# Kernel optimization log

Measured on AMD Instinct MI355X. Metric: run time of the kernel, lower is better.

Reference implementation:

```python
import jax, jax.numpy as jnp
import numpy as np

EPS = 1e-12

def _l2norm(v, axis):
    n = jnp.sqrt(jnp.sum(v * v, axis=axis, keepdims=True))
    return v / jnp.maximum(n, EPS)

def setup_inputs() -> dict:
    key = jax.random.key(0)
    k1, k2, k3, k4 = jax.random.split(key, 4)
    N, T, D, K = 8, 2048, 512, 64
    x = jax.random.normal(k1, (N, T, D), dtype=jnp.float32)
    W = jax.random.normal(k2, (K, D), dtype=jnp.float32) * (1.0 / np.sqrt(D))  # Conv1d(k=1) weight squeezed
    b = jax.random.normal(k3, (K,), dtype=jnp.float32) * 0.01
    centroids = jax.random.uniform(k4, (K, D), dtype=jnp.float32)
    return {"x": x, "W": W, "b": b, "centroids": centroids}

def reference(x, W, b, centroids):
    N, T, D = x.shape
    K = centroids.shape[0]
    # L2-normalize descriptors along feature dim
    xn = _l2norm(x, axis=2)                                  # [N,T,D]
    # Conv1d with kernel_size=1 == per-timestep linear: [N,K,T] logits over clusters
    logits = jnp.einsum('ntd,kd->nkt', xn, W) + b[None, :, None]
    a = jax.nn.softmax(logits, axis=1)                       # soft assignment over K
    # Algebraically equal to sum_t a[n,k,t] * (xn[n,t,:] - c[k,:])
    vlad = jnp.einsum('nkt,ntd->nkd', a, xn) \
         - jnp.sum(a, axis=2)[:, :, None] * centroids[None]  # [N,K,D]
    vlad = _l2norm(vlad, axis=2)                             # intra-normalize per cluster
    vlad = vlad.reshape(N, K * D)
    return _l2norm(vlad, axis=1)                             # global L2 normalize
```

## Files before the change

kernel.cpp:

```cpp
#include <hip/hip_runtime.h>
#include <math.h>

#define EPS 1e-12f
#define NN 8
#define TT 2048
#define DD 512
#define KK 64

typedef short short8 __attribute__((ext_vector_type(8)));
typedef float floatx4 __attribute__((ext_vector_type(4)));

__device__ __forceinline__ unsigned short f2bf(float f) {
    unsigned int u = __float_as_uint(f);
    u += 0x7FFFu + ((u >> 16) & 1u);
    return (unsigned short)(u >> 16);
}
__device__ __forceinline__ unsigned int pack2(float a, float b) {
    return (unsigned int)f2bf(a) | ((unsigned int)f2bf(b) << 16);
}


__global__ __launch_bounds__(256) void kA(const float* __restrict__ x,
                                          const float* __restrict__ W,
                                          const float* __restrict__ bias,
                                          unsigned short* __restrict__ xbT,
                                          unsigned short* __restrict__ aTs,
                                          float* __restrict__ asumP,
                                          float* __restrict__ norms) {
    __shared__ __align__(16) unsigned char smem[67584];
    unsigned short* sW = (unsigned short*)smem;
    unsigned short* sT = (unsigned short*)smem;
    float* sRed = (float*)(smem + 66560);

    const int tid = threadIdx.x;
    const int bid = blockIdx.x;
    const int w = tid >> 6, lane = tid & 63;
    const int l = lane & 15, q = lane >> 4;
    const int row0 = bid * 64 + w * 16;
    const int row = row0 + l;
    const int n = row0 >> 11;
    const int tl0 = row0 & (TT - 1);
    const int tblk = (bid * 64) & (TT - 1);

    const float* xr = x + (size_t)row * DD;
    short8 fragA[16];
    float ssq = 0.0f;
#pragma unroll
    for (int s = 0; s < 16; ++s) {
        float4 u0 = *(const float4*)(xr + s * 32 + q * 8);
        float4 u1 = *(const float4*)(xr + s * 32 + q * 8 + 4);
        ssq += u0.x*u0.x + u0.y*u0.y + u0.z*u0.z + u0.w*u0.w
             + u1.x*u1.x + u1.y*u1.y + u1.z*u1.z + u1.w*u1.w;
        uint4 pk;
        pk.x = pack2(u0.x, u0.y); pk.y = pack2(u0.z, u0.w);
        pk.z = pack2(u1.x, u1.y); pk.w = pack2(u1.z, u1.w);
        union { uint4 u; short8 s8; } cvt; cvt.u = pk;
        fragA[s] = cvt.s8;
    }

    {
        const int sp = tid >> 4, hp = (tid >> 2) & 3, qp = tid & 3;
        const float* wsrc = W + (size_t)(hp * 16) * DD + sp * 32 + qp * 8;
        unsigned short* wdst = sW + (size_t)tid * 128;
#pragma unroll
        for (int j = 0; j < 16; ++j) {
            float4 u0 = *(const float4*)(wsrc + (size_t)j * DD);
            float4 u1 = *(const float4*)(wsrc + (size_t)j * DD + 4);
            uint4 pk;
            pk.x = pack2(u0.x, u0.y); pk.y = pack2(u0.z, u0.w);
            pk.z = pack2(u1.x, u1.y); pk.w = pack2(u1.z, u1.w);
            *(uint4*)(wdst + j * 8) = pk;
        }
    }

    ssq += __shfl_xor(ssq, 16, 64);
    ssq += __shfl_xor(ssq, 32, 64);
    float st = 1.0f / fmaxf(sqrtf(ssq), EPS);

    __syncthreads();

    floatx4 acc[4];
#pragma unroll
    for (int h = 0; h < 4; ++h) acc[h] = floatx4{0.f, 0.f, 0.f, 0.f};
#pragma unroll
    for (int s = 0; s < 16; ++s) {
#pragma unroll
        for (int h = 0; h < 4; ++h) {
            short8 wf = *(const short8*)(sW + ((size_t)((s * 4 + h) * 64) + lane) * 8);
            acc[h] = __builtin_amdgcn_mfma_f32_16x16x32_bf16(fragA[s], wf, acc[h], 0, 0, 0);
        }
    }

    float sr[4];
#pragma unroll
    for (int r = 0; r < 4; ++r) sr[r] = __shfl(st, 4 * q + r, 64);
    float bj[4];
#pragma unroll
    for (int h = 0; h < 4; ++h) bj[h] = bias[h * 16 + l];

    float av[4][4];
#pragma unroll
    for (int r = 0; r < 4; ++r) {
        float v0 = acc[0][r] * sr[r] + bj[0], v1 = acc[1][r] * sr[r] + bj[1];
        float v2 = acc[2][r] * sr[r] + bj[2], v3 = acc[3][r] * sr[r] + bj[3];
        float m = fmaxf(fmaxf(v0, v1), fmaxf(v2, v3));
#pragma unroll
        for (int msk = 1; msk <= 8; msk <<= 1) m = fmaxf(m, __shfl_xor(m, msk, 64));
        float e0 = __expf(v0 - m), e1 = __expf(v1 - m), e2 = __expf(v2 - m), e3 = __expf(v3 - m);
        float ss = e0 + e1 + e2 + e3;
#pragma unroll
        for (int msk = 1; msk <= 8; msk <<= 1) ss += __shfl_xor(ss, msk, 64);
        float inv = 1.0f / ss;
        av[0][r] = e0 * inv; av[1][r] = e1 * inv; av[2][r] = e2 * inv; av[3][r] = e3 * inv;
    }

#pragma unroll
    for (int h = 0; h < 4; ++h) {
        uint2 p;
        p.x = pack2(av[h][0] * sr[0], av[h][1] * sr[1]);
        p.y = pack2(av[h][2] * sr[2], av[h][3] * sr[3]);
        *(uint2*)(aTs + ((size_t)(n * KK + h * 16 + l)) * TT + tl0 + 4 * q) = p;
    }

#pragma unroll
    for (int h = 0; h < 4; ++h) {
        float sh = av[h][0] + av[h][1] + av[h][2] + av[h][3];
        sh += __shfl_xor(sh, 16, 64);
        sh += __shfl_xor(sh, 32, 64);
        if (q == 0) sRed[w * 64 + h * 16 + l] = sh;
    }
    __syncthreads();
    if (tid < 64) {
        float s0 = sRed[tid] + sRed[64 + tid] + sRed[128 + tid] + sRed[192 + tid];
        asumP[(size_t)bid * 64 + tid] = s0;
    }

#pragma unroll
    for (int s = 0; s < 16; ++s)
        *(short8*)(sT + (size_t)(w * 16 + l) * 520 + s * 32 + q * 8) = fragA[s];
    __syncthreads();

#pragma unroll
    for (int c = 0; c < 2; ++c) {
        int d = tid + c * 256;
        const unsigned short* colb = sT + d;
        unsigned short* ob = xbT + ((size_t)(n * DD + d)) * TT + tblk;
#pragma unroll
        for (int jj = 0; jj < 8; ++jj) {
            uint4 pk;
            pk.x = (unsigned int)colb[(jj * 8 + 0) * 520] | ((unsigned int)colb[(jj * 8 + 1) * 520] << 16);
            pk.y = (unsigned int)colb[(jj * 8 + 2) * 520] | ((unsigned int)colb[(jj * 8 + 3) * 520] << 16);
            pk.z = (unsigned int)colb[(jj * 8 + 4) * 520] | ((unsigned int)colb[(jj * 8 + 5) * 520] << 16);
            pk.w = (unsigned int)colb[(jj * 8 + 6) * 520] | ((unsigned int)colb[(jj * 8 + 7) * 520] << 16);
            *(uint4*)(ob + jj * 8) = pk;
        }
    }

    if (bid == 0) { norms[tid] = 0.0f; norms[tid + 256] = 0.0f; }
}

__global__ __launch_bounds__(256) void kB(const unsigned short* __restrict__ xbT,
                                          const unsigned short* __restrict__ aTs,
                                          const float* __restrict__ asumP,
                                          const float* __restrict__ cent,
                                          float* __restrict__ vpre,
                                          float* __restrict__ norms) {
    __shared__ float sAs[16];
    const int tid = threadIdx.x;
    const int w = tid >> 6, lane = tid & 63;
    const int l = lane & 15, q = lane >> 4;
    const int bid = blockIdx.x;
    const int kq = bid >> 6, n = (bid >> 3) & 7, dq = bid & 7;
    const int k0 = kq * 16;
    const int dbase = dq * 64 + w * 16;

    if (tid < 16) sAs[tid] = 0.0f;
    __syncthreads();
    {
        const int kk = tid & 15, chunk = tid >> 4;
        float p = asumP[(size_t)(n * 32 + chunk) * 64 + k0 + kk]
                + asumP[(size_t)(n * 32 + 16 + chunk) * 64 + k0 + kk];
        p += __shfl_xor(p, 16, 64);
        p += __shfl_xor(p, 32, 64);
        if (q == 0) atomicAdd(&sAs[kk], p);
    }

    const unsigned short* ap = aTs + ((size_t)(n * KK + k0 + l)) * TT + q * 8;
    const unsigned short* bp = xbT + ((size_t)(n * DD + dbase + l)) * TT + q * 8;
    floatx4 a0 = {0.f, 0.f, 0.f, 0.f}, a1 = a0, a2 = a0, a3 = a0;
#pragma unroll
    for (int s = 0; s < 64; s += 4) {
        a0 = __builtin_amdgcn_mfma_f32_16x16x32_bf16(*(const short8*)(ap + (s + 0) * 32),
                                                     *(const short8*)(bp + (s + 0) * 32), a0, 0, 0, 0);
        a1 = __builtin_amdgcn_mfma_f32_16x16x32_bf16(*(const short8*)(ap + (s + 1) * 32),
                                                     *(const short8*)(bp + (s + 1) * 32), a1, 0, 0, 0);
        a2 = __builtin_amdgcn_mfma_f32_16x16x32_bf16(*(const short8*)(ap + (s + 2) * 32),
                                                     *(const short8*)(bp + (s + 2) * 32), a2, 0, 0, 0);
        a3 = __builtin_amdgcn_mfma_f32_16x16x32_bf16(*(const short8*)(ap + (s + 3) * 32),
                                                     *(const short8*)(bp + (s + 3) * 32), a3, 0, 0, 0);
    }
    floatx4 acc;
#pragma unroll
    for (int r = 0; r < 4; ++r) acc[r] = (a0[r] + a1[r]) + (a2[r] + a3[r]);

    __syncthreads();

    const int d = dbase + l;
#pragma unroll
    for (int r = 0; r < 4; ++r) {
        int k = k0 + 4 * q + r;
        float val = acc[r] - sAs[4 * q + r] * cent[(size_t)k * DD + d];
        vpre[((size_t)(n * KK + k)) * DD + d] = val;
        float s2 = val * val;
#pragma unroll
        for (int msk = 1; msk <= 8; msk <<= 1) s2 += __shfl_xor(s2, msk, 64);
        if (l == 0) atomicAdd(&norms[n * KK + k], s2);
    }
}

__global__ __launch_bounds__(128) void kC(const float* __restrict__ vpre,
                                          const float* __restrict__ norms,
                                          float* __restrict__ out) {
    const int nk = blockIdx.x;
    const int tid = threadIdx.x;
    float nr = sqrtf(norms[nk]);
    float sc = 1.0f / (fmaxf(nr, EPS) * 8.0f);
    float4 v4 = ((const float4*)(vpre + (size_t)nk * DD))[tid];
    v4.x *= sc; v4.y *= sc; v4.z *= sc; v4.w *= sc;
    ((float4*)(out + (size_t)nk * DD))[tid] = v4;
}

extern "C" void kernel_launch(void* const* d_in, const int* in_sizes, int n_in,
                              void* d_out, int out_size, void* d_ws, size_t ws_size,
                              hipStream_t stream) {
    const float* x    = (const float*)d_in[0];
    const float* W    = (const float*)d_in[1];
    const float* b    = (const float*)d_in[2];
    const float* cent = (const float*)d_in[3];
    float* out = (float*)d_out;

    float* w = (float*)d_ws;
    unsigned short* xbT = (unsigned short*)(w + 0);
    unsigned short* aTs = (unsigned short*)(w + 4194304);
    float* vpre  = w + 4718592;
    float* asumP = w + 4980736;
    float* norms = w + 4997120;

    hipLaunchKernelGGL(kA, dim3(256), dim3(256), 0, stream, x, W, b, xbT, aTs, asumP, norms);
    hipLaunchKernelGGL(kB, dim3(256), dim3(256), 0, stream, xbT, aTs, asumP, cent, vpre, norms);
    hipLaunchKernelGGL(kC, dim3(512), dim3(128), 0, stream, vpre, norms, out);
}
```

Before: 111.7 us.

## Store bf16 x row-major and transpose tiles in LDS inside aggregation kernel

kA now writes the normalized-input bf16 copy in its natural [N,T,D] layout directly from registers, dropping the LDS transpose and strided column stores. kB is restructured: 512 blocks each cover 32 clusters by 16 features, with the four waves splitting T into quarters. Each wave double-buffers swizzled LDS tiles of x to form MFMA B fragments, and the partial results are reduced across waves through shared memory. This aims to cut kA's transpose cost and improve kB parallelism, at the price of more LDS traffic and a cross-wave reduction in kB.

Measured after the change: 103.9 us. 6.9% less time.

```diff
diff --git a/kernel.cpp b/kernel.cpp
--- a/kernel.cpp
+++ b/kernel.cpp
@@ -23,14 +23,12 @@
 __global__ __launch_bounds__(256) void kA(const float* __restrict__ x,
                                           const float* __restrict__ W,
                                           const float* __restrict__ bias,
-                                          unsigned short* __restrict__ xbT,
+                                          unsigned short* __restrict__ xb,
                                           unsigned short* __restrict__ aTs,
                                           float* __restrict__ asumP,
                                           float* __restrict__ norms) {
-    __shared__ __align__(16) unsigned char smem[67584];
-    unsigned short* sW = (unsigned short*)smem;
-    unsigned short* sT = (unsigned short*)smem;
-    float* sRed = (float*)(smem + 66560);
+    __shared__ unsigned short sW[32768];
+    __shared__ float sRed[256];
 
     const int tid = threadIdx.x;
     const int bid = blockIdx.x;
@@ -40,9 +38,9 @@
     const int row = row0 + l;
     const int n = row0 >> 11;
     const int tl0 = row0 & (TT - 1);
-    const int tblk = (bid * 64) & (TT - 1);
 
     const float* xr = x + (size_t)row * DD;
+    unsigned short* xo = xb + (size_t)row * DD;
     short8 fragA[16];
     float ssq = 0.0f;
 #pragma unroll
@@ -56,6 +54,7 @@
         pk.z = pack2(u1.x, u1.y); pk.w = pack2(u1.z, u1.w);
         union { uint4 u; short8 s8; } cvt; cvt.u = pk;
         fragA[s] = cvt.s8;
+        *(uint4*)(xo + s * 32 + q * 8) = pk;
     }
 
     {
@@ -135,87 +134,93 @@
         asumP[(size_t)bid * 64 + tid] = s0;
     }
 
-#pragma unroll
-    for (int s = 0; s < 16; ++s)
-        *(short8*)(sT + (size_t)(w * 16 + l) * 520 + s * 32 + q * 8) = fragA[s];
-    __syncthreads();
-
-#pragma unroll
-    for (int c = 0; c < 2; ++c) {
-        int d = tid + c * 256;
-        const unsigned short* colb = sT + d;
-        unsigned short* ob = xbT + ((size_t)(n * DD + d)) * TT + tblk;
-#pragma unroll
-        for (int jj = 0; jj < 8; ++jj) {
-            uint4 pk;
-            pk.x = (unsigned int)colb[(jj * 8 + 0) * 520] | ((unsigned int)colb[(jj * 8 + 1) * 520] << 16);
-            pk.y = (unsigned int)colb[(jj * 8 + 2) * 520] | ((unsigned int)colb[(jj * 8 + 3) * 520] << 16);
-            pk.z = (unsigned int)colb[(jj * 8 + 4) * 520] | ((unsigned int)colb[(jj * 8 + 5) * 520] << 16);
-            pk.w = (unsigned int)colb[(jj * 8 + 6) * 520] | ((unsigned int)colb[(jj * 8 + 7) * 520] << 16);
-            *(uint4*)(ob + jj * 8) = pk;
-        }
-    }
-
     if (bid == 0) { norms[tid] = 0.0f; norms[tid + 256] = 0.0f; }
 }
 
-__global__ __launch_bounds__(256) void kB(const unsigned short* __restrict__ xbT,
+__global__ __launch_bounds__(256) void kB(const unsigned short* __restrict__ xb,
                                           const unsigned short* __restrict__ aTs,
                                           const float* __restrict__ asumP,
                                           const float* __restrict__ cent,
                                           float* __restrict__ vpre,
                                           float* __restrict__ norms) {
-    __shared__ float sAs[16];
+    __shared__ __align__(16) unsigned short sX[4][2][1024];
+    __shared__ float sC[4][512];
+    __shared__ float sAs[32];
+
     const int tid = threadIdx.x;
     const int w = tid >> 6, lane = tid & 63;
     const int l = lane & 15, q = lane >> 4;
     const int bid = blockIdx.x;
-    const int kq = bid >> 6, n = (bid >> 3) & 7, dq = bid & 7;
-    const int k0 = kq * 16;
-    const int dbase = dq * 64 + w * 16;
-
-    if (tid < 16) sAs[tid] = 0.0f;
+    const int n = bid & 7, dt = (bid >> 3) & 31, kh = bid >> 8;
+    const int k0 = kh * 32;
+    const int d0 = dt * 16;
+
+    float myAsum = 0.0f;
+    if (tid < 32) {
+#pragma unroll 16
+        for (int c = 0; c < 32; ++c)
+            myAsum += asumP[(size_t)(n * 32 + c) * 64 + k0 + tid];
+    }
+
+    const int tq0 = w * 512;
+    const unsigned short* xbase = xb + ((size_t)(n * TT + tq0 + lane)) * DD + d0;
+    const unsigned short* ap = aTs + ((size_t)(n * KK + k0 + l)) * TT + tq0 + q * 8;
+    unsigned short* b0 = &sX[w][0][0];
+    unsigned short* b1 = &sX[w][1][0];
+    const int gsw = lane & 7;
+
+#define STAGE(S, BUF)                                                          \
+    {                                                                          \
+        const unsigned short* p_ = xbase + (size_t)(S) * 64 * DD;              \
+        unsigned short vals[16];                                               \
+        *(uint4*)(vals) = *(const uint4*)(p_);                                 \
+        *(uint4*)(vals + 8) = *(const uint4*)(p_ + 8);                         \
+        _Pragma("unroll")                                                      \
+        for (int e = 0; e < 16; ++e)                                           \
+            (BUF)[e * 64 + ((((lane >> 3) ^ (e & 7))) << 3) + (lane & 7)] = vals[e]; \
+    }
+
+    floatx4 acc0 = {0.f, 0.f, 0.f, 0.f}, acc1 = acc0;
+
+    STAGE(0, b0);
+#pragma unroll
+    for (int s = 0; s < 8; ++s) {
+        unsigned short* cur = (s & 1) ? b1 : b0;
+        unsigned short* nxt = (s & 1) ? b0 : b1;
+        if (s < 7) STAGE(s + 1, nxt);
+#pragma unroll
+        for (int ks = 0; ks < 2; ++ks) {
+            short8 bf = *(const short8*)(cur + ((l & 15) * 64 + ((((ks << 2) + q) ^ gsw) << 3)));
+            short8 a0 = *(const short8*)(ap + s * 64 + ks * 32);
+            short8 a1 = *(const short8*)(ap + 16 * TT + s * 64 + ks * 32);
+            acc0 = __builtin_amdgcn_mfma_f32_16x16x32_bf16(a0, bf, acc0, 0, 0, 0);
+            acc1 = __builtin_amdgcn_mfma_f32_16x16x32_bf16(a1, bf, acc1, 0, 0, 0);
+        }
+    }
+#undef STAGE
+
+#pragma unroll
+    for (int r = 0; r < 4; ++r) {
+        sC[w][(4 * q + r) * 16 + l] = acc0[r];
+        sC[w][(16 + 4 * q + r) * 16 + l] = acc1[r];
+    }
+    if (tid < 32) sAs[tid] = myAsum;
     __syncthreads();
-    {
-        const int kk = tid & 15, chunk = tid >> 4;
-        float p = asumP[(size_t)(n * 32 + chunk) * 64 + k0 + kk]
-                + asumP[(size_t)(n * 32 + 16 + chunk) * 64 + k0 + kk];
-        p += __shfl_xor(p, 16, 64);
-        p += __shfl_xor(p, 32, 64);
-        if (q == 0) atomicAdd(&sAs[kk], p);
-    }
-
-    const unsigned short* ap = aTs + ((size_t)(n * KK + k0 + l)) * TT + q * 8;
-    const unsigned short* bp = xbT + ((size_t)(n * DD + dbase + l)) * TT + q * 8;
-    floatx4 a0 = {0.f, 0.f, 0.f, 0.f}, a1 = a0, a2 = a0, a3 = a0;
-#pragma unroll
-    for (int s = 0; s < 64; s += 4) {
-        a0 = __builtin_amdgcn_mfma_f32_16x16x32_bf16(*(const short8*)(ap + (s + 0) * 32),
-                                                     *(const short8*)(bp + (s + 0) * 32), a0, 0, 0, 0);
-        a1 = __builtin_amdgcn_mfma_f32_16x16x32_bf16(*(const short8*)(ap + (s + 1) * 32),
-                                                     *(const short8*)(bp + (s + 1) * 32), a1, 0, 0, 0);
-        a2 = __builtin_amdgcn_mfma_f32_16x16x32_bf16(*(const short8*)(ap + (s + 2) * 32),
-                                                     *(const short8*)(bp + (s + 2) * 32), a2, 0, 0, 0);
-        a3 = __builtin_amdgcn_mfma_f32_16x16x32_bf16(*(const short8*)(ap + (s + 3) * 32),
-                                                     *(const short8*)(bp + (s + 3) * 32), a3, 0, 0, 0);
-    }
-    floatx4 acc;
-#pragma unroll
-    for (int r = 0; r < 4; ++r) acc[r] = (a0[r] + a1[r]) + (a2[r] + a3[r]);
-
-    __syncthreads();
-
-    const int d = dbase + l;
-#pragma unroll
-    for (int r = 0; r < 4; ++r) {
-        int k = k0 + 4 * q + r;
-        float val = acc[r] - sAs[4 * q + r] * cent[(size_t)k * DD + d];
-        vpre[((size_t)(n * KK + k)) * DD + d] = val;
-        float s2 = val * val;
-#pragma unroll
-        for (int msk = 1; msk <= 8; msk <<= 1) s2 += __shfl_xor(s2, msk, 64);
-        if (l == 0) atomicAdd(&norms[n * KK + k], s2);
-    }
+
+    const int e0 = tid * 2;
+    const int kl = e0 >> 4, d = e0 & 15;
+    float v0 = (sC[0][e0] + sC[1][e0]) + (sC[2][e0] + sC[3][e0]);
+    float v1 = (sC[0][e0 + 1] + sC[1][e0 + 1]) + (sC[2][e0 + 1] + sC[3][e0 + 1]);
+    float as = sAs[kl];
+    const float* cp = cent + (size_t)(k0 + kl) * DD + d0 + d;
+    v0 -= as * cp[0];
+    v1 -= as * cp[1];
+    *(float2*)(vpre + ((size_t)(n * KK + k0 + kl)) * DD + d0 + d) = make_float2(v0, v1);
+    float s2 = v0 * v0 + v1 * v1;
+    s2 += __shfl_xor(s2, 1, 64);
+    s2 += __shfl_xor(s2, 2, 64);
+    s2 += __shfl_xor(s2, 4, 64);
+    if ((tid & 7) == 0) atomicAdd(&norms[n * KK + k0 + kl], s2);
 }
 
 __global__ __launch_bounds__(128) void kC(const float* __restrict__ vpre,
@@ -240,13 +245,13 @@
     float* out = (float*)d_out;
 
     float* w = (float*)d_ws;
-    unsigned short* xbT = (unsigned short*)(w + 0);
+    unsigned short* xb  = (unsigned short*)(w + 0);
     unsigned short* aTs = (unsigned short*)(w + 4194304);
     float* vpre  = w + 4718592;
     float* asumP = w + 4980736;
     float* norms = w + 4997120;
 
-    hipLaunchKernelGGL(kA, dim3(256), dim3(256), 0, stream, x, W, b, xbT, aTs, asumP, norms);
-    hipLaunchKernelGGL(kB, dim3(256), dim3(256), 0, stream, xbT, aTs, asumP, cent, vpre, norms);
+    hipLaunchKernelGGL(kA, dim3(256), dim3(256), 0, stream, x, W, b, xb, aTs, asumP, norms);
+    hipLaunchKernelGGL(kB, dim3(512), dim3(256), 0, stream, xb, aTs, asumP, cent, vpre, norms);
     hipLaunchKernelGGL(kC, dim3(512), dim3(128), 0, stream, vpre, norms, out);
 }
```
